# Kernel tuning notes

Hardware: AMD Instinct MI355X
Metric: run time of the kernel (lower is better)

Reference implementation:

```python
import jax, jax.numpy as jnp
import numpy as np

N_NODES = 100000
N_EDGES = 1600000
DIM = 64
N_REL = 8
N_LAYERS = 2


def setup_inputs() -> dict:
    key = jax.random.key(0)
    ks = jax.random.split(key, 6)
    x = jax.random.normal(ks[0], (N_NODES, DIM), dtype=jnp.float32)
    weight = jax.random.normal(ks[1], (N_LAYERS, N_REL, DIM, DIM), dtype=jnp.float32) * (1.0 / np.sqrt(DIM))
    root = jax.random.normal(ks[2], (N_LAYERS, DIM, DIM), dtype=jnp.float32) * (1.0 / np.sqrt(DIM))
    bias = jnp.zeros((N_LAYERS, DIM), dtype=jnp.float32)
    edge_index = jax.random.randint(ks[3], (2, N_EDGES), 0, N_NODES, dtype=jnp.int32)
    edge_type = jax.random.randint(ks[4], (N_EDGES,), 0, N_REL, dtype=jnp.int32)
    return {"x": x, "weight": weight, "root": root, "bias": bias,
            "edge_index": edge_index, "edge_type": edge_type}


def _rgcn_layer(x, W, W_root, b, src, dst, edge_type, num_nodes, num_rel):
    # Per-relation node transform: [R, N, F] (equivalent to per-edge W[etype] @ x_src)
    h = jnp.einsum('nd,rdf->rnf', x, W)
    msg = h[edge_type, src]  # [E, F] relation-indexed gather
    # FastRGCNConv 'mean' aggregation: normalize by per-(dst, relation) edge count
    comb = dst * num_rel + edge_type
    cnt = jax.ops.segment_sum(jnp.ones(src.shape, dtype=x.dtype), comb,
                              num_segments=num_nodes * num_rel)
    norm = 1.0 / jnp.clip(cnt[comb], 1.0)
    agg = jax.ops.segment_sum(msg * norm[:, None], dst, num_segments=num_nodes)
    return agg + x @ W_root + b


def reference(x, weight, root, bias, edge_index, edge_type):
    src, dst = edge_index[0], edge_index[1]
    num_nodes = x.shape[0]
    num_rel = weight.shape[1]
    for l in range(weight.shape[0]):  # stacked RGCN layers, no nonlinearity (as in source)
        x = _rgcn_layer(x, weight[l], root[l], bias[l], src, dst, edge_type,
                        num_nodes, num_rel)
    return x
```

## Files before the change

### kernel.cpp

```cpp
#include <hip/hip_runtime.h>

#define NN    100000
#define NE    1600000
#define DIM   64
#define NREL  8
#define NSEG  (NN * NREL)
#define NTOT  (NSEG + 1)
#define CHUNK 1024
#define NBLK  ((NTOT + CHUNK - 1) / CHUNK)
#define KTOT  (9 * DIM)
#define KAGG  (8 * DIM)
#define APAD  (KTOT + 8)
#define APAD2 (KAGG + 8)
#define ESPMAX (NE + NSEG)
#define SEGB  2048
#define NBUCK ((NSEG + SEGB - 1) / SEGB)

typedef unsigned short bf16u;
using short8  = __attribute__((ext_vector_type(8))) short;
using bfx4    = __attribute__((ext_vector_type(4))) unsigned short;
using f32x4   = __attribute__((ext_vector_type(4))) float;
using float4v = __attribute__((ext_vector_type(4))) float;

#if defined(__has_builtin)
#if __has_builtin(__builtin_amdgcn_make_buffer_rsrc) && \
    __has_builtin(__builtin_amdgcn_raw_buffer_load_b32) && \
    __has_builtin(__builtin_amdgcn_raw_buffer_store_b32)
#define HAVE_BUF 1
#endif
#endif

#ifdef HAVE_BUF
__device__ __forceinline__ __amdgpu_buffer_rsrc_t mk_rsrc(const void* p, unsigned bytes) {
    return __builtin_amdgcn_make_buffer_rsrc(const_cast<void*>(p), (short)0,
                                             (int)bytes, 0x00020000);
}
#endif

__device__ __forceinline__ bf16u f2bf(float v) {
    unsigned b = __float_as_uint(v);
    return (bf16u)((b + 0x7FFFu + ((b >> 16) & 1u)) >> 16);
}
__device__ __forceinline__ float bf2f(bf16u u) {
    return __uint_as_float((unsigned)u << 16);
}

__device__ __forceinline__ int block_exscan(int v, int* lds) {
    int tid = threadIdx.x;
    lds[tid] = v;
    __syncthreads();
    for (int s = 1; s < (int)blockDim.x; s <<= 1) {
        int t = (tid >= s) ? lds[tid - s] : 0;
        __syncthreads();
        lds[tid] += t;
        __syncthreads();
    }
    return lds[tid] - v;
}

__global__ __launch_bounds__(256) void bcount_k(const int* __restrict__ dst,
                                                const int* __restrict__ et,
                                                int* __restrict__ bcnt) {
    __shared__ int bl[NBUCK];
    for (int i = threadIdx.x; i < NBUCK; i += 256) bl[i] = 0;
    __syncthreads();
    const int base = blockIdx.x * 4096;
#pragma unroll
    for (int j = 0; j < 16; ++j) {
        int i = base + j * 256 + threadIdx.x;
        if (i < NE) atomicAdd(&bl[(dst[i] * NREL + et[i]) >> 11], 1);
    }
    __syncthreads();
    for (int i = threadIdx.x; i < NBUCK; i += 256)
        if (bl[i]) atomicAdd(&bcnt[i], bl[i]);
}

__global__ __launch_bounds__(512) void bscan_k(const int* __restrict__ bcnt,
                                               int* __restrict__ bstart,
                                               int* __restrict__ bcur) {
    __shared__ int lds[512];
    int v = (threadIdx.x < NBUCK) ? bcnt[threadIdx.x] : 0;
    int e = block_exscan(v, lds);
    if (threadIdx.x < NBUCK) { bstart[threadIdx.x] = e; bcur[threadIdx.x] = e; }
    if (threadIdx.x == NBUCK - 1) bstart[NBUCK] = e + v;
}

__global__ __launch_bounds__(256) void part1_k(const int* __restrict__ src,
                                               const int* __restrict__ dst,
                                               const int* __restrict__ et,
                                               int* __restrict__ bcur,
                                               int* __restrict__ tmp_src,
                                               int* __restrict__ tmp_c) {
    __shared__ int cntl[NBUCK];
    __shared__ int basel[NBUCK];
    for (int i = threadIdx.x; i < NBUCK; i += 256) cntl[i] = 0;
    __syncthreads();
    const int base = blockIdx.x * 2048;
    int cs[8], rs[8], ss[8];
#pragma unroll
    for (int j = 0; j < 8; ++j) {
        int i = base + j * 256 + threadIdx.x;
        cs[j] = -1;
        if (i < NE) {
            cs[j] = dst[i] * NREL + et[i];
            ss[j] = src[i];
            rs[j] = atomicAdd(&cntl[cs[j] >> 11], 1);
        }
    }
    __syncthreads();
    for (int i = threadIdx.x; i < NBUCK; i += 256)
        basel[i] = cntl[i] ? atomicAdd(&bcur[i], cntl[i]) : 0;
    __syncthreads();
#pragma unroll
    for (int j = 0; j < 8; ++j)
        if (cs[j] >= 0) {
            int p = basel[cs[j] >> 11] + rs[j];
            tmp_src[p] = ss[j];
            tmp_c[p]   = cs[j];
        }
}

__global__ __launch_bounds__(256) void ncount_k(const int* __restrict__ tmp_c,
                                                const int* __restrict__ bstart,
                                                int* __restrict__ cnt) {
    __shared__ int rk[SEGB];
    const int b = blockIdx.x, c0 = b * SEGB;
    const int nsb = min(SEGB, NSEG - c0);
    for (int i = threadIdx.x; i < SEGB; i += 256) rk[i] = 0;
    __syncthreads();
    const int e0 = bstart[b], e1 = bstart[b + 1];
    for (int e = e0 + threadIdx.x; e < e1; e += 256)
        atomicAdd(&rk[tmp_c[e] - c0], 1);
    __syncthreads();
    for (int i = threadIdx.x; i < nsb; i += 256) cnt[c0 + i] = rk[i];
}

__global__ __launch_bounds__(256) void part2_k(const int* __restrict__ tmp_src,
                                               const int* __restrict__ tmp_c,
                                               const int* __restrict__ bstart,
                                               const int* __restrict__ offp,
                                               int* __restrict__ esp) {
    __shared__ int rk[SEGB];
    const int b = blockIdx.x, c0 = b * SEGB;
    for (int i = threadIdx.x; i < SEGB; i += 256) rk[i] = 0;
    __syncthreads();
    const int e0 = bstart[b], e1 = bstart[b + 1];
    for (int e = e0 + threadIdx.x; e < e1; e += 256) {
        int c = tmp_c[e];
        int r = atomicAdd(&rk[c - c0], 1);
        esp[offp[c] + r] = tmp_src[e];
    }
}

__global__ __launch_bounds__(256) void count_k(const int* __restrict__ dst,
                                               const int* __restrict__ et,
                                               int* __restrict__ cnt, int E) {
    int i = blockIdx.x * 256 + threadIdx.x;
    if (i < E) atomicAdd(&cnt[dst[i] * NREL + et[i]], 1);
}

__global__ __launch_bounds__(256) void scanA_p(const int* __restrict__ cnt,
                                               int* __restrict__ bsum) {
    __shared__ int lds[256];
    int base = blockIdx.x * CHUNK + threadIdx.x * 4;
    int s = 0;
#pragma unroll
    for (int j = 0; j < 4; ++j) {
        int i = base + j;
        if (i < NSEG) { int v = cnt[i]; s += v + (v & 1); }
    }
    int e = block_exscan(s, lds);
    if (threadIdx.x == 255) bsum[blockIdx.x] = e + s;
}

__global__ __launch_bounds__(1024) void scanB(int* __restrict__ bsum) {
    __shared__ int lds[1024];
    int v = (threadIdx.x < NBLK) ? bsum[threadIdx.x] : 0;
    int e = block_exscan(v, lds);
    if (threadIdx.x < NBLK) bsum[threadIdx.x] = e;
}

__global__ __launch_bounds__(256) void scanC_p(const int* __restrict__ cnt,
                                               const int* __restrict__ bsum,
                                               int* __restrict__ offp,
                                               float* __restrict__ inv,
                                               int* __restrict__ esp) {
    __shared__ int lds[256];
    int base = blockIdx.x * CHUNK + threadIdx.x * 4;
    int c4[4], v4[4]; int s = 0;
#pragma unroll
    for (int j = 0; j < 4; ++j) {
        int i = base + j;
        c4[j] = (i < NSEG) ? cnt[i] : 0;
        v4[j] = c4[j] + (c4[j] & 1);
        s += v4[j];
    }
    int e = block_exscan(s, lds) + bsum[blockIdx.x];
#pragma unroll
    for (int j = 0; j < 4; ++j) {
        int i = base + j;
        if (i < NSEG) {
            offp[i] = e;
            inv[i]  = (c4[j] > 0) ? 1.0f / (float)c4[j] : 0.0f;
            if (c4[j] & 1) esp[e + c4[j]] = NN;
            e += v4[j];
        } else if (i == NSEG) { offp[i] = e; }
    }
}

__global__ __launch_bounds__(256) void scanA(const int* __restrict__ cnt,
                                             int* __restrict__ bsum) {
    __shared__ int lds[256];
    int base = blockIdx.x * CHUNK + threadIdx.x * 4;
    int s = 0;
#pragma unroll
    for (int j = 0; j < 4; ++j) { int i = base + j; if (i < NSEG) s += cnt[i]; }
    int e = block_exscan(s, lds);
    if (threadIdx.x == 255) bsum[blockIdx.x] = e + s;
}

__global__ __launch_bounds__(256) void scanC(const int* __restrict__ cnt,
                                             const int* __restrict__ bsum,
                                             int* __restrict__ off,
                                             int* __restrict__ cur) {
    __shared__ int lds[256];
    int base = blockIdx.x * CHUNK + threadIdx.x * 4;
    int v[4]; int s = 0;
#pragma unroll
    for (int j = 0; j < 4; ++j) { int i = base + j; v[j] = (i < NSEG) ? cnt[i] : 0; s += v[j]; }
    int e = block_exscan(s, lds) + bsum[blockIdx.x];
#pragma unroll
    for (int j = 0; j < 4; ++j) {
        int i = base + j;
        if (i < NSEG)       { off[i] = e; cur[i] = e; e += v[j]; }
        else if (i == NSEG) { off[i] = e; }
    }
}

__global__ __launch_bounds__(256) void scatter_k(const int* __restrict__ src,
                                                 const int* __restrict__ dst,
                                                 const int* __restrict__ et,
                                                 int* __restrict__ cur,
                                                 int* __restrict__ es, int E) {
    int i = blockIdx.x * 256 + threadIdx.x;
    if (i < E) {
        int c = dst[i] * NREL + et[i];
        int p = atomicAdd(&cur[c], 1);
        es[p] = src[i];
    }
}

__global__ __launch_bounds__(256) void xcvt_k(const float* __restrict__ x,
                                              bf16u* __restrict__ xb) {
    int i = blockIdx.x * 256 + threadIdx.x;
    int e4 = i * 4;
    if (e4 < NN * DIM) {
        float4v v = *(const float4v*)(x + e4);
        bfx4 o;
        o.x = f2bf(v.x); o.y = f2bf(v.y); o.z = f2bf(v.z); o.w = f2bf(v.w);
        *(bfx4*)(xb + e4) = o;
    } else if (e4 < (NN + 1) * DIM) {
        bfx4 z = {0, 0, 0, 0};
        *(bfx4*)(xb + e4) = z;
    }
}

__global__ __launch_bounds__(64) void zrow_k(bf16u* __restrict__ xb1) {
    xb1[(size_t)NN * DIM + threadIdx.x] = 0;
}

__global__ __launch_bounds__(256) void btk(const float* __restrict__ W,
                                           const float* __restrict__ R,
                                           bf16u* __restrict__ BtG) {
    int idx = blockIdx.x * 256 + threadIdx.x;
    if (idx >= 2 * DIM * KTOT) return;
    int k = idx % KTOT;
    int n = (idx / KTOT) & (DIM - 1);
    int l = idx / (KTOT * DIM);
    float v;
    if (k < 8 * DIM) v = W[(((size_t)l * NREL + (k >> 6)) * DIM + (k & 63)) * DIM + n];
    else             v = R[((size_t)l * DIM + (k - 8 * DIM)) * DIM + n];
    BtG[idx] = f2bf(v);
}

__global__ __launch_bounds__(256, 8) void agg2_k(
    const bf16u* __restrict__ xb, const int* __restrict__ offp,
    const float* __restrict__ invf, const int* __restrict__ esp,
    bf16u* __restrict__ Ag)
{
    const int lane = threadIdx.x & 63;
    const int wv   = threadIdx.x >> 6;
    const int d0   = (blockIdx.x * 4 + wv) * 8;
    if (d0 >= NN) return;
    const int c0 = d0 * NREL;

#ifdef HAVE_BUF
    const __amdgpu_buffer_rsrc_t xrsrc = mk_rsrc(xb,  (unsigned)((NN + 1) * DIM * 2));
    const __amdgpu_buffer_rsrc_t ersrc = mk_rsrc(esp, (unsigned)(ESPMAX * 4));
    const __amdgpu_buffer_rsrc_t arsrc = mk_rsrc(Ag,  0xFFFFFFFFu);
    const int xoff4 = (lane & 31) * 4;
#define ESLD(pos)  (int)__builtin_amdgcn_raw_buffer_load_b32(ersrc, (pos) * 4, 0, 0)
#define XLD(sv)    __builtin_amdgcn_raw_buffer_load_b32(xrsrc, ((sv) << 7) + xoff4, 0, 0)
#define AGST(pk, seg)                                                          \
    if (lane < 32)                                                             \
        __builtin_amdgcn_raw_buffer_store_b32((pk), arsrc, (lane & 31) * 4,    \
            ((d0 + ((seg) >> 3)) * KAGG + ((seg) & 7) * DIM) * 2, 0);
#else
#define ESLD(pos)  esp[min((pos), ESPMAX - 1)]
#define XLD(sv)    (*(const unsigned*)(xb + (size_t)(sv) * DIM + (lane & 31) * 2))
#define AGST(pk, seg)                                                          \
    if (lane < 32)                                                             \
        *(unsigned*)(Ag + ((size_t)(d0 + ((seg) >> 3)) * KAGG                  \
                           + ((seg) & 7) * DIM + (lane & 31) * 2)) = (pk);
#endif

    int offv = offp[c0 + 1 + lane];
    int invv = ((const int*)invf)[c0 + lane];
    int pBase = __builtin_amdgcn_readfirstlane(offp[c0]);
    int pEnd  = __builtin_amdgcn_readlane(offv, 63);

    int idsbase = pBase;
    int ids = ESLD(idsbase + lane);

    unsigned q0 = 0, q1 = 0, q2 = 0, q3 = 0, q4 = 0, q5 = 0, q6 = 0, q7 = 0;
    {
        int pf = pBase;
#define PRIME(Q) if (pf < pEnd) {                                             \
        int idx = pf - idsbase;                                               \
        int sv0 = __builtin_amdgcn_readlane(ids, idx);                        \
        int sv1 = __builtin_amdgcn_readlane(ids, idx + 1);                    \
        int sv  = (lane < 32) ? sv0 : sv1;                                    \
        Q = XLD(sv); }                                                        \
        pf += 2;
        PRIME(q0) PRIME(q1) PRIME(q2) PRIME(q3)
        PRIME(q4) PRIME(q5) PRIME(q6) PRIME(q7)
#undef PRIME
    }
    int seg = 0, p = pBase;
    int se      = __builtin_amdgcn_readlane(offv, 0);
    float invn  = __int_as_float(__builtin_amdgcn_readlane(invv, 0));
    float accA = 0.f, accB = 0.f;

#define STEP(Q) {                                                             \
        while (p == se) {             \
            float ta = accA + __shfl_xor(accA, 32);                           \
            float tb = accB + __shfl_xor(accB, 32);                           \
            unsigned pk = (unsigned)f2bf(ta * invn)                           \
                        | ((unsigned)f2bf(tb * invn) << 16);                  \
            AGST(pk, seg)                                                     \
            accA = 0.f; accB = 0.f;                                           \
            if (++seg >= 64) goto agg_done;                                   \
            se   = __builtin_amdgcn_readlane(offv, seg);                      \
            invn = __int_as_float(__builtin_amdgcn_readlane(invv, seg));      \
        }                                                                     \
        accA += __uint_as_float(Q << 16);                                     \
        accB += __uint_as_float(Q & 0xffff0000u);                             \
        int pn = p + 16;                                                      \
        if (pn < pEnd) {                                                      \
            int idx = pn - idsbase;                                           \
            if (idx >= 64) { idsbase = pn;                                    \
                ids = ESLD(idsbase + lane); idx = 0; }                        \
            int sv0 = __builtin_amdgcn_readlane(ids, idx);                    \
            int sv1 = __builtin_amdgcn_readlane(ids, idx + 1);                \
            int sv  = (lane < 32) ? sv0 : sv1;                                \
            Q = XLD(sv);                                                      \
        }                                                                     \
        p += 2; }

    for (;;) { STEP(q0) STEP(q1) STEP(q2) STEP(q3)
               STEP(q4) STEP(q5) STEP(q6) STEP(q7) }
agg_done: ;
#undef STEP
#undef ESLD
#undef XLD
#undef AGST
}

template<bool BF16OUT>
__global__ __launch_bounds__(512, 4) void gemm2_k(
    const bf16u* __restrict__ Ag, const bf16u* __restrict__ xb,
    const bf16u* __restrict__ BtG, const float* __restrict__ bias,
    void* __restrict__ outv)
{
    __shared__ bf16u A[64 * APAD2];
    const int tid  = threadIdx.x;
    const int base = blockIdx.x * 64;

    {
        const int srow = tid >> 3, scg = tid & 7;
        const bf16u* gsrc = Ag + (size_t)min(base + srow, NN - 1) * KAGG + scg * 8;
        bf16u* ldst = &A[srow * APAD2 + scg * 8];
#pragma unroll
        for (int j = 0; j < 8; ++j)
            *(short8*)(ldst + j * 64) = *(const short8*)(gsrc + j * 64);
    }
    __syncthreads();

    const int lane = tid & 63, wv = tid >> 6;
    const int l15 = lane & 15, hw = lane >> 4;
    const int tid0 = wv * 2;
    const int tm = tid0 >> 2, tn0 = tid0 & 3;
    const bf16u* Arow = &A[(tm * 16 + l15) * APAD2 + hw * 8];
    const bf16u* xrow = xb + (size_t)min(base + tm * 16 + l15, NN - 1) * DIM + hw * 8;
    const bf16u* B0   = &BtG[(size_t)(tn0 * 16 + l15) * KTOT + hw * 8];
    const bf16u* B1   = B0 + 16 * KTOT;
    f32x4 acc0 = {0.f, 0.f, 0.f, 0.f}, acc1 = {0.f, 0.f, 0.f, 0.f};
#pragma unroll
    for (int ks = 0; ks < KTOT / 32; ++ks) {
        short8 af = (ks < 16) ? *(const short8*)(Arow + ks * 32)
                              : *(const short8*)(xrow + (ks - 16) * 32);
        short8 b0 = *(const short8*)(B0 + ks * 32);
        short8 b1 = *(const short8*)(B1 + ks * 32);
        acc0 = __builtin_amdgcn_mfma_f32_16x16x32_bf16(af, b0, acc0, 0, 0, 0);
        acc1 = __builtin_amdgcn_mfma_f32_16x16x32_bf16(af, b1, acc1, 0, 0, 0);
    }
    int col0 = tn0 * 16 + l15;
    int r0   = tm * 16 + hw * 4;
    float bv0 = bias[col0], bv1 = bias[col0 + 16];
#pragma unroll
    for (int j = 0; j < 4; ++j) {
        int row = base + r0 + j;
        if (row < NN) {
            if constexpr (BF16OUT) {
                bf16u* out = (bf16u*)outv;
                out[(size_t)row * DIM + col0]      = f2bf(acc0[j] + bv0);
                out[(size_t)row * DIM + col0 + 16] = f2bf(acc1[j] + bv1);
            } else {
                float* out = (float*)outv;
                out[(size_t)row * DIM + col0]      = acc0[j] + bv0;
                out[(size_t)row * DIM + col0 + 16] = acc1[j] + bv1;
            }
        }
    }
}

__global__ __launch_bounds__(512, 4) void layer_k(
    const float* __restrict__ xin, const bf16u* __restrict__ BtG,
    const float* __restrict__ bias, const int* __restrict__ off,
    const int* __restrict__ es, float* __restrict__ out)
{
    __shared__ bf16u A[64 * APAD];
    const int lane = threadIdx.x & 63;
    const int wv   = threadIdx.x >> 6;
    const int base = blockIdx.x * 64;
    const int d0   = base + wv * 8;
    const int nds  = min(8, NN - d0);
    bf16u* Aw = &A[wv * 8 * APAD];

    if (nds > 0) {
        const int c0   = d0 * NREL;
        const int nseg = nds * NREL;
        int s1v = off[min(c0 + lane + 1, NSEG)];
        int pBase = off[min(c0, NSEG)];
        pBase = __builtin_amdgcn_readfirstlane(pBase);
        int pEnd  = __builtin_amdgcn_readlane(s1v, nseg - 1);

        float xroot[8];
#pragma unroll
        for (int i = 0; i < 8; ++i)
            xroot[i] = xin[(size_t)min(d0 + i, NN - 1) * DIM + lane];

        int idsbase = pBase;
        int ids = es[min(idsbase + lane, NE - 1)];

        float q0 = 0.f, q1 = 0.f, q2 = 0.f, q3 = 0.f,
              q4 = 0.f, q5 = 0.f, q6 = 0.f, q7 = 0.f;
        {
            int pf = pBase;
#define PRIME(Q) if (pf < pEnd) { int idx = pf - idsbase;                     \
        int sv = __builtin_amdgcn_readlane(ids, idx);                         \
        Q = xin[(size_t)sv * DIM + lane]; } ++pf;
            PRIME(q0) PRIME(q1) PRIME(q2) PRIME(q3)
            PRIME(q4) PRIME(q5) PRIME(q6) PRIME(q7)
#undef PRIME
        }
        int seg = 0, segStart = pBase, p = pBase;
        int se = __builtin_amdgcn_readlane(s1v, 0);
        float acc = 0.f;

#define STEP(Q) {                                                             \
        while (p == se) {                                                     \
            int n = se - segStart;                                            \
            float invn = (n > 0) ? 1.0f / (float)n : 0.f;                     \
            Aw[(seg >> 3) * APAD + (seg & 7) * DIM + lane] = f2bf(acc * invn);\
            acc = 0.f; segStart = p;                                          \
            if (++seg >= nseg) goto agg_done;                                 \
            se = __builtin_amdgcn_readlane(s1v, seg);                         \
        }                                                                     \
        acc += Q;                                                             \
        int pn = p + 8;                                                       \
        if (pn < pEnd) {                                                      \
            int idx = pn - idsbase;                                           \
            if (idx >= 64) { idsbase = pn;                                    \
                ids = es[min(idsbase + lane, NE - 1)]; idx = 0; }             \
            int sv = __builtin_amdgcn_readlane(ids, idx);                     \
            Q = xin[(size_t)sv * DIM + lane];                                 \
        }                                                                     \
        ++p; }

        for (;;) { STEP(q0) STEP(q1) STEP(q2) STEP(q3)
                   STEP(q4) STEP(q5) STEP(q6) STEP(q7) }
agg_done: ;
#undef STEP

#pragma unroll
        for (int i = 0; i < 8; ++i) {
            if (i < nds) Aw[i * APAD + 8 * DIM + lane] = f2bf(xroot[i]);
            else {
#pragma unroll
                for (int r = 0; r < 9; ++r) Aw[i * APAD + r * DIM + lane] = 0;
            }
        }
    } else {
#pragma unroll
        for (int i = 0; i < 8; ++i)
#pragma unroll
            for (int r = 0; r < 9; ++r) Aw[i * APAD + r * DIM + lane] = 0;
    }
    __syncthreads();

    const int l15 = lane & 15, hw = lane >> 4;
    const int tid0 = wv * 2;
    const int tm = tid0 >> 2, tn0 = tid0 & 3;
    const bf16u* Arow = &A[(tm * 16 + l15) * APAD + hw * 8];
    const bf16u* B0   = &BtG[(size_t)(tn0 * 16 + l15) * KTOT + hw * 8];
    const bf16u* B1   = B0 + 16 * KTOT;
    f32x4 acc0 = {0.f, 0.f, 0.f, 0.f}, acc1 = {0.f, 0.f, 0.f, 0.f};
#pragma unroll
    for (int ks = 0; ks < KTOT / 32; ++ks) {
        short8 af = *(const short8*)(Arow + ks * 32);
        short8 b0 = *(const short8*)(B0 + ks * 32);
        short8 b1 = *(const short8*)(B1 + ks * 32);
        acc0 = __builtin_amdgcn_mfma_f32_16x16x32_bf16(af, b0, acc0, 0, 0, 0);
        acc1 = __builtin_amdgcn_mfma_f32_16x16x32_bf16(af, b1, acc1, 0, 0, 0);
    }
    int col0 = tn0 * 16 + l15;
    int r0   = tm * 16 + hw * 4;
    float bv0 = bias[col0], bv1 = bias[col0 + 16];
#pragma unroll
    for (int j = 0; j < 4; ++j) {
        int row = base + r0 + j;
        if (row < NN) {
            out[(size_t)row * DIM + col0]      = acc0[j] + bv0;
            out[(size_t)row * DIM + col0 + 16] = acc1[j] + bv1;
        }
    }
}

__global__ __launch_bounds__(256) void root_k(const float* __restrict__ x,
                                              const float* __restrict__ R,
                                              const float* __restrict__ b,
                                              float* __restrict__ out, int N) {
    int wid  = (blockIdx.x * 256 + threadIdx.x) >> 6;
    int lane = threadIdx.x & 63;
    if (wid >= N) return;
    wid = __builtin_amdgcn_readfirstlane(wid);
    const float* xs = x + (size_t)wid * DIM;
    float acc = b[lane];
#pragma unroll
    for (int k = 0; k < DIM; ++k)
        acc = fmaf(xs[k], R[k * DIM + lane], acc);
    out[(size_t)wid * DIM + lane] = acc;
}

__global__ __launch_bounds__(256) void edge_k(const float* __restrict__ x,
                                              const float* __restrict__ W,
                                              const int* __restrict__ srcv,
                                              const int* __restrict__ dstv,
                                              const int* __restrict__ etv,
                                              const int* __restrict__ cnt,
                                              float* __restrict__ out, int E) {
    int wid  = (blockIdx.x * 256 + threadIdx.x) >> 6;
    int lane = threadIdx.x & 63;
    if (wid >= E) return;
    int s = __builtin_amdgcn_readfirstlane(srcv[wid]);
    int d = __builtin_amdgcn_readfirstlane(dstv[wid]);
    int t = __builtin_amdgcn_readfirstlane(etv[wid]);
    const float* xs = x + (size_t)s * DIM;
    const float* w  = W + (size_t)t * DIM * DIM;
    float acc = 0.f;
#pragma unroll
    for (int k = 0; k < DIM; ++k)
        acc = fmaf(xs[k], w[k * DIM + lane], acc);
    float nrm = 1.0f / fmaxf((float)cnt[d * NREL + t], 1.0f);
    atomicAdd(&out[(size_t)d * DIM + lane], acc * nrm);
}

extern "C" void kernel_launch(void* const* d_in, const int* in_sizes, int n_in,
                              void* d_out, int out_size, void* d_ws, size_t ws_size,
                              hipStream_t stream) {
    const float* x  = (const float*)d_in[0];
    const float* W  = (const float*)d_in[1];
    const float* R  = (const float*)d_in[2];
    const float* B  = (const float*)d_in[3];
    const int*   ei = (const int*)d_in[4];
    const int*   et = (const int*)d_in[5];
    const int* src = ei;
    const int* dst = ei + NE;
    float* out = (float*)d_out;
    char* ws = (char*)d_ws;

    const size_t BIG_WS  = 144160000;
    const size_t FAST_WS = 41604096;

    if (ws_size >= BIG_WS) {
        bf16u* xb0  = (bf16u*)(ws + 0);
        bf16u* xb1  = (bf16u*)(ws + 12800256);
        int*   offp = (int*)  (ws + 25600512);
        float* inv  = (float*)(ws + 28800528);
        int*   esp  = (int*)  (ws + 32000544);
        bf16u* Ag   = (bf16u*)(ws + 41600544);
        int*   cnt     = (int*)(ws + 41600544);
        int*   tmp_src = (int*)(ws + 44800544);
        int*   tmp_c   = (int*)(ws + 51200544);
        bf16u* BtG  = (bf16u*)(ws + 144000544);
        int*   bsum = (int*)  (ws + 144148000);
        int*   bcnt = (int*)  (ws + 144151168);
        int*   bstart=(int*)  (ws + 144152768);
        int*   bcur = (int*)  (ws + 144154368);

        hipMemsetAsync(bcnt, 0, sizeof(int) * (NBUCK + 1), stream);
        bcount_k<<<(NE + 4095) / 4096, 256, 0, stream>>>(dst, et, bcnt);
        bscan_k<<<1, 512, 0, stream>>>(bcnt, bstart, bcur);
        part1_k<<<(NE + 2047) / 2048, 256, 0, stream>>>(src, dst, et, bcur, tmp_src, tmp_c);
        ncount_k<<<NBUCK, 256, 0, stream>>>(tmp_c, bstart, cnt);
        scanA_p<<<NBLK, 256, 0, stream>>>(cnt, bsum);
        scanB<<<1, 1024, 0, stream>>>(bsum);
        scanC_p<<<NBLK, 256, 0, stream>>>(cnt, bsum, offp, inv, esp);
        part2_k<<<NBUCK, 256, 0, stream>>>(tmp_src, tmp_c, bstart, offp, esp);
        btk<<<(2 * DIM * KTOT + 255) / 256, 256, 0, stream>>>(W, R, BtG);
        xcvt_k<<<((NN + 1) * DIM / 4 + 255) / 256, 256, 0, stream>>>(x, xb0);
        zrow_k<<<1, 64, 0, stream>>>(xb1);

        int gblk = (NN + 63) / 64;
        int ablk = NN / 32;
        agg2_k<<<ablk, 256, 0, stream>>>(xb0, offp, inv, esp, Ag);
        gemm2_k<true ><<<gblk, 512, 0, stream>>>(Ag, xb0, BtG, B, (void*)xb1);
        agg2_k<<<ablk, 256, 0, stream>>>(xb1, offp, inv, esp, Ag);
        gemm2_k<false><<<gblk, 512, 0, stream>>>(Ag, xb1, BtG + DIM * KTOT, B + DIM, (void*)out);
    } else if (ws_size >= FAST_WS) {
        float* x1  = (float*)(ws + 0);
        int*   cnt = (int*)  (ws + 25600000);
        int*   off = (int*)  (ws + 28800000);
        int*   cur = (int*)  (ws + 32000016);
        int*   es  = (int*)  (ws + 35200016);
        int*   bsum= (int*)  (ws + 41600016);
        bf16u* BtG = (bf16u*)(ws + 32000016);

        hipMemsetAsync(cnt, 0, sizeof(int) * NSEG, stream);
        count_k<<<(NE + 255) / 256, 256, 0, stream>>>(dst, et, cnt, NE);
        scanA<<<NBLK, 256, 0, stream>>>(cnt, bsum);
        scanB<<<1, 1024, 0, stream>>>(bsum);
        scanC<<<NBLK, 256, 0, stream>>>(cnt, bsum, off, cur);
        scatter_k<<<(NE + 255) / 256, 256, 0, stream>>>(src, dst, et, cur, es, NE);
        btk<<<(2 * DIM * KTOT + 255) / 256, 256, 0, stream>>>(W, R, BtG);

        int nblk = (NN + 63) / 64;
        layer_k<<<nblk, 512, 0, stream>>>(x,  BtG,              B,       off, es, x1);
        layer_k<<<nblk, 512, 0, stream>>>(x1, BtG + DIM * KTOT, B + DIM, off, es, out);
    } else {
        float* x1  = (float*)ws;
        int*   cnt = (int*)(ws + 25600000);
        hipMemsetAsync(cnt, 0, sizeof(int) * NSEG, stream);
        count_k<<<(NE + 255) / 256, 256, 0, stream>>>(dst, et, cnt, NE);
        root_k<<<(NN * 64) / 256 + 1, 256, 0, stream>>>(x, R, B, x1, NN);
        edge_k<<<(NE * 64) / 256, 256, 0, stream>>>(x, W, src, dst, et, cnt, x1, NE);
        root_k<<<(NN * 64) / 256 + 1, 256, 0, stream>>>(x1, R + DIM * DIM, B + DIM, out, NN);
        edge_k<<<(NE * 64) / 256, 256, 0, stream>>>(x1, W + NREL * DIM * DIM, src, dst, et, cnt, out, NE);
    }
}
```

Measured before the change: 430.1 us.

## Pack src and local segment into one word, deepen gather prefetch, drop zrow kernel

Each bucketed edge now goes into a single 32-bit word holding the source id shifted left by 11 and the 11-bit local segment index, replacing two separate int arrays. This halves the temporary write and read traffic in the partition, count and second-partition kernels. The aggregation gather loop doubles its register prefetch depth from 8 to 16 outstanding row loads to hide more latency, at the cost of extra registers. The separate zero-row kernel is folded into the conversion kernel, removing one launch.

```diff
diff --git a/kernel.cpp b/kernel.cpp
--- a/kernel.cpp
+++ b/kernel.cpp
@@ -89,21 +89,20 @@
                                                const int* __restrict__ dst,
                                                const int* __restrict__ et,
                                                int* __restrict__ bcur,
-                                               int* __restrict__ tmp_src,
-                                               int* __restrict__ tmp_c) {
+                                               unsigned* __restrict__ tmp) {
     __shared__ int cntl[NBUCK];
     __shared__ int basel[NBUCK];
     for (int i = threadIdx.x; i < NBUCK; i += 256) cntl[i] = 0;
     __syncthreads();
     const int base = blockIdx.x * 2048;
-    int cs[8], rs[8], ss[8];
+    int cs[8], rs[8]; unsigned pw[8];
 #pragma unroll
     for (int j = 0; j < 8; ++j) {
         int i = base + j * 256 + threadIdx.x;
         cs[j] = -1;
         if (i < NE) {
             cs[j] = dst[i] * NREL + et[i];
-            ss[j] = src[i];
+            pw[j] = ((unsigned)src[i] << 11) | ((unsigned)cs[j] & 2047u);
             rs[j] = atomicAdd(&cntl[cs[j] >> 11], 1);
         }
     }
@@ -113,14 +112,11 @@
     __syncthreads();
 #pragma unroll
     for (int j = 0; j < 8; ++j)
-        if (cs[j] >= 0) {
-            int p = basel[cs[j] >> 11] + rs[j];
-            tmp_src[p] = ss[j];
-            tmp_c[p]   = cs[j];
-        }
-}
-
-__global__ __launch_bounds__(256) void ncount_k(const int* __restrict__ tmp_c,
+        if (cs[j] >= 0)
+            tmp[basel[cs[j] >> 11] + rs[j]] = pw[j];
+}
+
+__global__ __launch_bounds__(256) void ncount_k(const unsigned* __restrict__ tmp,
                                                 const int* __restrict__ bstart,
                                                 int* __restrict__ cnt) {
     __shared__ int rk[SEGB];
@@ -130,13 +126,12 @@
     __syncthreads();
     const int e0 = bstart[b], e1 = bstart[b + 1];
     for (int e = e0 + threadIdx.x; e < e1; e += 256)
-        atomicAdd(&rk[tmp_c[e] - c0], 1);
+        atomicAdd(&rk[tmp[e] & 2047u], 1);
     __syncthreads();
     for (int i = threadIdx.x; i < nsb; i += 256) cnt[c0 + i] = rk[i];
 }
 
-__global__ __launch_bounds__(256) void part2_k(const int* __restrict__ tmp_src,
-                                               const int* __restrict__ tmp_c,
+__global__ __launch_bounds__(256) void part2_k(const unsigned* __restrict__ tmp,
                                                const int* __restrict__ bstart,
                                                const int* __restrict__ offp,
                                                int* __restrict__ esp) {
@@ -146,9 +141,10 @@
     __syncthreads();
     const int e0 = bstart[b], e1 = bstart[b + 1];
     for (int e = e0 + threadIdx.x; e < e1; e += 256) {
-        int c = tmp_c[e];
-        int r = atomicAdd(&rk[c - c0], 1);
-        esp[offp[c] + r] = tmp_src[e];
+        unsigned w = tmp[e];
+        int lc = (int)(w & 2047u);
+        int r = atomicAdd(&rk[lc], 1);
+        esp[offp[c0 + lc] + r] = (int)(w >> 11);
     }
 }
 
@@ -251,7 +247,8 @@
 }
 
 __global__ __launch_bounds__(256) void xcvt_k(const float* __restrict__ x,
-                                              bf16u* __restrict__ xb) {
+                                              bf16u* __restrict__ xb,
+                                              bf16u* __restrict__ xb1) {
     int i = blockIdx.x * 256 + threadIdx.x;
     int e4 = i * 4;
     if (e4 < NN * DIM) {
@@ -261,12 +258,9 @@
         *(bfx4*)(xb + e4) = o;
     } else if (e4 < (NN + 1) * DIM) {
         bfx4 z = {0, 0, 0, 0};
-        *(bfx4*)(xb + e4) = z;
-    }
-}
-
-__global__ __launch_bounds__(64) void zrow_k(bf16u* __restrict__ xb1) {
-    xb1[(size_t)NN * DIM + threadIdx.x] = 0;
+        *(bfx4*)(xb + e4)  = z;
+        *(bfx4*)(xb1 + e4) = z;
+    }
 }
 
 __global__ __launch_bounds__(256) void btk(const float* __restrict__ W,
@@ -322,7 +316,8 @@
     int idsbase = pBase;
     int ids = ESLD(idsbase + lane);
 
-    unsigned q0 = 0, q1 = 0, q2 = 0, q3 = 0, q4 = 0, q5 = 0, q6 = 0, q7 = 0;
+    unsigned q0 = 0, q1 = 0, q2 = 0, q3 = 0, q4 = 0, q5 = 0, q6 = 0, q7 = 0,
+             q8 = 0, q9 = 0, qa = 0, qb = 0, qc = 0, qd = 0, qe = 0, qf = 0;
     {
         int pf = pBase;
 #define PRIME(Q) if (pf < pEnd) {                                             \
@@ -334,6 +329,8 @@
         pf += 2;
         PRIME(q0) PRIME(q1) PRIME(q2) PRIME(q3)
         PRIME(q4) PRIME(q5) PRIME(q6) PRIME(q7)
+        PRIME(q8) PRIME(q9) PRIME(qa) PRIME(qb)
+        PRIME(qc) PRIME(qd) PRIME(qe) PRIME(qf)
 #undef PRIME
     }
     int seg = 0, p = pBase;
@@ -355,7 +352,7 @@
         }                                                                     \
         accA += __uint_as_float(Q << 16);                                     \
         accB += __uint_as_float(Q & 0xffff0000u);                             \
-        int pn = p + 16;                                                      \
+        int pn = p + 32;                                                      \
         if (pn < pEnd) {                                                      \
             int idx = pn - idsbase;                                           \
             if (idx >= 64) { idsbase = pn;                                    \
@@ -368,7 +365,9 @@
         p += 2; }
 
     for (;;) { STEP(q0) STEP(q1) STEP(q2) STEP(q3)
-               STEP(q4) STEP(q5) STEP(q6) STEP(q7) }
+               STEP(q4) STEP(q5) STEP(q6) STEP(q7)
+               STEP(q8) STEP(q9) STEP(qa) STEP(qb)
+               STEP(qc) STEP(qd) STEP(qe) STEP(qf) }
 agg_done: ;
 #undef STEP
 #undef ESLD
@@ -610,9 +609,8 @@
         float* inv  = (float*)(ws + 28800528);
         int*   esp  = (int*)  (ws + 32000544);
         bf16u* Ag   = (bf16u*)(ws + 41600544);
-        int*   cnt     = (int*)(ws + 41600544);
-        int*   tmp_src = (int*)(ws + 44800544);
-        int*   tmp_c   = (int*)(ws + 51200544);
+        int*      cnt = (int*)     (ws + 41600544);
+        unsigned* tmp = (unsigned*)(ws + 44800544);
         bf16u* BtG  = (bf16u*)(ws + 144000544);
         int*   bsum = (int*)  (ws + 144148000);
         int*   bcnt = (int*)  (ws + 144151168);
@@ -622,15 +620,14 @@
         hipMemsetAsync(bcnt, 0, sizeof(int) * (NBUCK + 1), stream);
         bcount_k<<<(NE + 4095) / 4096, 256, 0, stream>>>(dst, et, bcnt);
         bscan_k<<<1, 512, 0, stream>>>(bcnt, bstart, bcur);
-        part1_k<<<(NE + 2047) / 2048, 256, 0, stream>>>(src, dst, et, bcur, tmp_src, tmp_c);
-        ncount_k<<<NBUCK, 256, 0, stream>>>(tmp_c, bstart, cnt);
+        part1_k<<<(NE + 2047) / 2048, 256, 0, stream>>>(src, dst, et, bcur, tmp);
+        ncount_k<<<NBUCK, 256, 0, stream>>>(tmp, bstart, cnt);
         scanA_p<<<NBLK, 256, 0, stream>>>(cnt, bsum);
         scanB<<<1, 1024, 0, stream>>>(bsum);
         scanC_p<<<NBLK, 256, 0, stream>>>(cnt, bsum, offp, inv, esp);
-        part2_k<<<NBUCK, 256, 0, stream>>>(tmp_src, tmp_c, bstart, offp, esp);
+        part2_k<<<NBUCK, 256, 0, stream>>>(tmp, bstart, offp, esp);
         btk<<<(2 * DIM * KTOT + 255) / 256, 256, 0, stream>>>(W, R, BtG);
-        xcvt_k<<<((NN + 1) * DIM / 4 + 255) / 256, 256, 0, stream>>>(x, xb0);
-        zrow_k<<<1, 64, 0, stream>>>(xb1);
+        xcvt_k<<<((NN + 1) * DIM / 4 + 255) / 256, 256, 0, stream>>>(x, xb0, xb1);
 
         int gblk = (NN + 63) / 64;
         int ablk = NN / 32;
```

Measured after the change: 407.1 us. 5.3% less time.
